# Kernel tuning notes

Hardware: AMD Instinct MI355X
Metric: run time of the kernel (lower is better)

Reference implementation:

```python
import jax, jax.numpy as jnp
import numpy as np

BN_EPS = 1e-5

def setup_inputs() -> dict:
    key = jax.random.key(0)
    ks = jax.random.split(key, 6)
    N, D, H = 1024, 256, 128
    scale = 0.05
    return {
        "graph_embeddings": jax.random.normal(ks[0], (N, D), jnp.float32),
        "W1": jax.random.normal(ks[1], (2 * D, H), jnp.float32) * scale,
        "b1": jnp.zeros((H,), jnp.float32),
        "W2": jax.random.normal(ks[2], (H, 1), jnp.float32) * scale,
        "b2": jnp.zeros((1,), jnp.float32),
        "Wg": jax.random.normal(ks[3], (D, H), jnp.float32) * scale,
        "bg": jnp.zeros((H,), jnp.float32),
        "gamma": jnp.ones((H,), jnp.float32),
        "beta": jnp.zeros((H,), jnp.float32),
    }

def reference(graph_embeddings, W1, b1, W2, b2, Wg, bg, gamma, beta):
    N, D = graph_embeddings.shape
    # Pairwise similarity MLP: sim(i,j) = sigmoid(W2 @ relu(W1 @ [x_i; x_j] + b1) + b2)
    # Split W1 over the concat dim so we never materialize [N,N,2D].
    a = graph_embeddings @ W1[:D]          # [N, H] contribution of x_i
    c = graph_embeddings @ W1[D:]          # [N, H] contribution of x_j
    h = jax.nn.relu(a[:, None, :] + c[None, :, :] + b1)   # [N, N, H]
    sim = jax.nn.sigmoid(jnp.einsum('ijh,h->ij', h, W2[:, 0]) + b2[0])  # [N, N]
    # Torch loop uses sim(i,j) with i<j for both directions; keep edge iff sim > 0.5.
    U = jnp.triu(sim, k=1)
    A = jnp.where(U > 0.5, U, 0.0)
    A = A + A.T + jnp.eye(N, dtype=sim.dtype)  # symmetric + GCN self-loops (weight 1)
    # GCN symmetric normalization: D^{-1/2} A D^{-1/2}
    deg = A.sum(axis=1)
    dis = jax.lax.rsqrt(deg)
    A_hat = A * dis[:, None] * dis[None, :]
    out = A_hat @ (graph_embeddings @ Wg) + bg  # [N, H]
    # BatchNorm1d (training mode: batch stats, biased variance)
    mean = out.mean(axis=0)
    var = out.var(axis=0)
    out = gamma * (out - mean) * jax.lax.rsqrt(var + BN_EPS) + beta
    return jax.nn.relu(out)
```

## Files before the change

kernel.cpp:

```cpp
#include <hip/hip_runtime.h>
#include <math.h>

constexpr int NN = 1024;
constexpr int DD = 256;
constexpr int HH = 128;
constexpr float BN_EPS = 1e-5f;

constexpr int OFF_A      = 0;
constexpr int OFF_AP     = OFF_A + NN * NN;
constexpr int OFF_CP     = OFF_AP + NN * HH;
constexpr int OFF_Y      = OFF_CP + NN * HH;
constexpr int OFF_DEG    = OFF_Y + NN * HH;
constexpr int OFF_STATS  = OFF_DEG + NN;
constexpr int OFF_OUTPRE = OFF_STATS + 256;

__global__ __launch_bounds__(256) void k1_gemm(
    const float* __restrict__ X, const float* __restrict__ W1,
    const float* __restrict__ Wg, const float* __restrict__ b1,
    float* __restrict__ aP, float* __restrict__ cP, float* __restrict__ Y,
    float* __restrict__ deg, float* __restrict__ stats) {
  const int tid = threadIdx.x;
  const int blk = blockIdx.x;
  if (blk >= 192) {
    if (blk == 192) {
      for (int i = tid; i < NN; i += 256) deg[i] = 0.f;
    } else {
      stats[tid] = 0.f;
    }
    return;
  }
  __shared__ float xs[16 * 256];
  __shared__ float ws[64 * 128];
  const int i0 = (blk & 63) * 16;
  const int m = blk >> 6;
  const float* W = (m == 0) ? W1 : (m == 1 ? W1 + DD * HH : Wg);
  const float* Xbase = X + i0 * DD;
#pragma unroll
  for (int v = 0; v < 4; ++v) {
    const int fi = (v * 256 + tid) * 4;
    *(float4*)(xs + fi) = *(const float4*)(Xbase + fi);
  }
  const int tx = tid & 31, ty = tid >> 5;
  float4 acc0 = make_float4(0.f, 0.f, 0.f, 0.f);
  float4 acc1 = make_float4(0.f, 0.f, 0.f, 0.f);
  for (int c = 0; c < 4; ++c) {
    __syncthreads();
    const float* Wbase = W + c * 64 * HH;
#pragma unroll
    for (int v = 0; v < 8; ++v) {
      const int fi = (v * 256 + tid) * 4;
      *(float4*)(ws + fi) = *(const float4*)(Wbase + fi);
    }
    __syncthreads();
    const float* xr0 = xs + (ty * 2) * 256 + c * 64;
    const float* xr1 = xs + (ty * 2 + 1) * 256 + c * 64;
#pragma unroll 4
    for (int d = 0; d < 64; d += 4) {
      const float4 x0 = *(const float4*)(xr0 + d);
      const float4 x1 = *(const float4*)(xr1 + d);
      const float4 w0 = *(const float4*)(ws + (d + 0) * 128 + tx * 4);
      const float4 w1 = *(const float4*)(ws + (d + 1) * 128 + tx * 4);
      const float4 w2 = *(const float4*)(ws + (d + 2) * 128 + tx * 4);
      const float4 w3 = *(const float4*)(ws + (d + 3) * 128 + tx * 4);
      acc0.x = fmaf(x0.x, w0.x, acc0.x); acc0.y = fmaf(x0.x, w0.y, acc0.y);
      acc0.z = fmaf(x0.x, w0.z, acc0.z); acc0.w = fmaf(x0.x, w0.w, acc0.w);
      acc1.x = fmaf(x1.x, w0.x, acc1.x); acc1.y = fmaf(x1.x, w0.y, acc1.y);
      acc1.z = fmaf(x1.x, w0.z, acc1.z); acc1.w = fmaf(x1.x, w0.w, acc1.w);
      acc0.x = fmaf(x0.y, w1.x, acc0.x); acc0.y = fmaf(x0.y, w1.y, acc0.y);
      acc0.z = fmaf(x0.y, w1.z, acc0.z); acc0.w = fmaf(x0.y, w1.w, acc0.w);
      acc1.x = fmaf(x1.y, w1.x, acc1.x); acc1.y = fmaf(x1.y, w1.y, acc1.y);
      acc1.z = fmaf(x1.y, w1.z, acc1.z); acc1.w = fmaf(x1.y, w1.w, acc1.w);
      acc0.x = fmaf(x0.z, w2.x, acc0.x); acc0.y = fmaf(x0.z, w2.y, acc0.y);
      acc0.z = fmaf(x0.z, w2.z, acc0.z); acc0.w = fmaf(x0.z, w2.w, acc0.w);
      acc1.x = fmaf(x1.z, w2.x, acc1.x); acc1.y = fmaf(x1.z, w2.y, acc1.y);
      acc1.z = fmaf(x1.z, w2.z, acc1.z); acc1.w = fmaf(x1.z, w2.w, acc1.w);
      acc0.x = fmaf(x0.w, w3.x, acc0.x); acc0.y = fmaf(x0.w, w3.y, acc0.y);
      acc0.z = fmaf(x0.w, w3.z, acc0.z); acc0.w = fmaf(x0.w, w3.w, acc0.w);
      acc1.x = fmaf(x1.w, w3.x, acc1.x); acc1.y = fmaf(x1.w, w3.y, acc1.y);
      acc1.z = fmaf(x1.w, w3.z, acc1.z); acc1.w = fmaf(x1.w, w3.w, acc1.w);
    }
  }
  float* dst = (m == 0) ? aP : (m == 1 ? cP : Y);
  if (m == 0) {
    const float4 bv = *(const float4*)(b1 + tx * 4);
    acc0.x += bv.x; acc0.y += bv.y; acc0.z += bv.z; acc0.w += bv.w;
    acc1.x += bv.x; acc1.y += bv.y; acc1.z += bv.z; acc1.w += bv.w;
  }
  const int r0 = i0 + ty * 2;
  *(float4*)(dst + r0 * HH + tx * 4) = acc0;
  *(float4*)(dst + (r0 + 1) * HH + tx * 4) = acc1;
}

__global__ __launch_bounds__(256) void k2_pairwise(
    const float* __restrict__ aP, const float* __restrict__ cP,
    const float* __restrict__ W2, const float* __restrict__ b2,
    float* __restrict__ A, float* __restrict__ deg) {
  __shared__ float as[32 * 132];
  __shared__ float cs[32 * 132];
  __shared__ float es[32 * 33];
  __shared__ float ws2[128];
  const int tid = threadIdx.x;
  int tt = blockIdx.x, ti = 0;
  while (tt >= 32 - ti) { tt -= 32 - ti; ++ti; }
  const int tj = ti + tt;
  const int i0 = ti * 32, j0 = tj * 32;
  if (tid < 32) *(float4*)(ws2 + tid * 4) = *(const float4*)(W2 + tid * 4);
  for (int idx = tid; idx < 32 * HH; idx += 256) {
    const int row = idx >> 7, col = idx & 127;
    as[row * 132 + col] = aP[(i0 + row) * HH + col];
    cs[row * 132 + col] = cP[(j0 + row) * HH + col];
  }
  __syncthreads();
  const int li0 = (tid >> 4) * 2, lj0 = (tid & 15) * 2;
  float s00 = 0.f, s01 = 0.f, s10 = 0.f, s11 = 0.f;
#pragma unroll 8
  for (int h = 0; h < HH; h += 4) {
    const float4 a0 = *(const float4*)(as + li0 * 132 + h);
    const float4 a1 = *(const float4*)(as + (li0 + 1) * 132 + h);
    const float4 c0 = *(const float4*)(cs + lj0 * 132 + h);
    const float4 c1 = *(const float4*)(cs + (lj0 + 1) * 132 + h);
    const float4 w = *(const float4*)(ws2 + h);
    s00 += fmaxf(a0.x + c0.x, 0.f) * w.x + fmaxf(a0.y + c0.y, 0.f) * w.y +
           fmaxf(a0.z + c0.z, 0.f) * w.z + fmaxf(a0.w + c0.w, 0.f) * w.w;
    s01 += fmaxf(a0.x + c1.x, 0.f) * w.x + fmaxf(a0.y + c1.y, 0.f) * w.y +
           fmaxf(a0.z + c1.z, 0.f) * w.z + fmaxf(a0.w + c1.w, 0.f) * w.w;
    s10 += fmaxf(a1.x + c0.x, 0.f) * w.x + fmaxf(a1.y + c0.y, 0.f) * w.y +
           fmaxf(a1.z + c0.z, 0.f) * w.z + fmaxf(a1.w + c0.w, 0.f) * w.w;
    s11 += fmaxf(a1.x + c1.x, 0.f) * w.x + fmaxf(a1.y + c1.y, 0.f) * w.y +
           fmaxf(a1.z + c1.z, 0.f) * w.z + fmaxf(a1.w + c1.w, 0.f) * w.w;
  }
  const float b2v = b2[0];
  auto edge = [b2v](float s) {
    s += b2v;
    return s > 0.f ? 1.f / (1.f + __expf(-s)) : 0.f;
  };
  es[(li0 + 0) * 33 + lj0 + 0] = edge(s00);
  es[(li0 + 0) * 33 + lj0 + 1] = edge(s01);
  es[(li0 + 1) * 33 + lj0 + 0] = edge(s10);
  es[(li0 + 1) * 33 + lj0 + 1] = edge(s11);
  __syncthreads();
  if (ti == tj) {
    float f[2][2];
#pragma unroll
    for (int r = 0; r < 2; ++r)
#pragma unroll
      for (int c = 0; c < 2; ++c) {
        const int li = li0 + r, lj = lj0 + c;
        f[r][c] =
            (li == lj) ? 1.f : (li < lj ? es[li * 33 + lj] : es[lj * 33 + li]);
      }
    __syncthreads();
    es[(li0 + 0) * 33 + lj0 + 0] = f[0][0];
    es[(li0 + 0) * 33 + lj0 + 1] = f[0][1];
    es[(li0 + 1) * 33 + lj0 + 0] = f[1][0];
    es[(li0 + 1) * 33 + lj0 + 1] = f[1][1];
    __syncthreads();
  }
  if (tid < 32) {
    float s = 0.f;
#pragma unroll
    for (int c = 0; c < 32; ++c) s += es[tid * 33 + c];
    atomicAdd(deg + i0 + tid, s);
  } else if (tid < 64 && ti != tj) {
    const int c = tid - 32;
    float s = 0.f;
#pragma unroll
    for (int r = 0; r < 32; ++r) s += es[r * 33 + c];
    atomicAdd(deg + j0 + c, s);
  }
#pragma unroll
  for (int r = 0; r < 2; ++r)
#pragma unroll
    for (int c = 0; c < 2; ++c) {
      const int li = li0 + r, lj = lj0 + c;
      A[(i0 + li) * NN + j0 + lj] = es[li * 33 + lj];
      if (ti != tj) A[(j0 + li) * NN + i0 + lj] = es[lj * 33 + li];
    }
}

__global__ __launch_bounds__(256) void k3_spmm(
    const float* __restrict__ A, const float* __restrict__ Y,
    const float* __restrict__ deg, const float* __restrict__ bg,
    float* __restrict__ out_pre, float* __restrict__ stats) {
  __shared__ float Ast[NN * 4];
  __shared__ float disl[NN];
  __shared__ float red[8 * 520];
  __shared__ float sm1[256], sm2[256];
  const int tid = threadIdx.x;
  const int i0 = blockIdx.x * 4;
  {
    const float4 dv = *(const float4*)(deg + tid * 4);
    float4 r;
    r.x = rsqrtf(dv.x); r.y = rsqrtf(dv.y);
    r.z = rsqrtf(dv.z); r.w = rsqrtf(dv.w);
    *(float4*)(disl + tid * 4) = r;
  }
  __syncthreads();
  const float* Ab = A + i0 * NN;
#pragma unroll
  for (int v = 0; v < 4; ++v) {
    const int fi = (v * 256 + tid) * 4;
    const float4 av = *(const float4*)(Ab + fi);
    const int r = fi >> 10, j = fi & 1023;
    Ast[(j + 0) * 4 + r] = av.x * disl[j + 0];
    Ast[(j + 1) * 4 + r] = av.y * disl[j + 1];
    Ast[(j + 2) * 4 + r] = av.z * disl[j + 2];
    Ast[(j + 3) * 4 + r] = av.w * disl[j + 3];
  }
  __syncthreads();
  const int tx = tid & 31, ty = tid >> 5;
  const int jbase = ty * 128;
  float4 acc[4];
#pragma unroll
  for (int r = 0; r < 4; ++r) acc[r] = make_float4(0.f, 0.f, 0.f, 0.f);
  const float* Yb = Y + jbase * HH + tx * 4;
#pragma unroll 4
  for (int jj = 0; jj < 128; ++jj) {
    const float4 yv = *(const float4*)(Yb + jj * HH);
    const float4 ab = *(const float4*)(Ast + (jbase + jj) * 4);
    acc[0].x = fmaf(ab.x, yv.x, acc[0].x); acc[0].y = fmaf(ab.x, yv.y, acc[0].y);
    acc[0].z = fmaf(ab.x, yv.z, acc[0].z); acc[0].w = fmaf(ab.x, yv.w, acc[0].w);
    acc[1].x = fmaf(ab.y, yv.x, acc[1].x); acc[1].y = fmaf(ab.y, yv.y, acc[1].y);
    acc[1].z = fmaf(ab.y, yv.z, acc[1].z); acc[1].w = fmaf(ab.y, yv.w, acc[1].w);
    acc[2].x = fmaf(ab.z, yv.x, acc[2].x); acc[2].y = fmaf(ab.z, yv.y, acc[2].y);
    acc[2].z = fmaf(ab.z, yv.z, acc[2].z); acc[2].w = fmaf(ab.z, yv.w, acc[2].w);
    acc[3].x = fmaf(ab.w, yv.x, acc[3].x); acc[3].y = fmaf(ab.w, yv.y, acc[3].y);
    acc[3].z = fmaf(ab.w, yv.z, acc[3].z); acc[3].w = fmaf(ab.w, yv.w, acc[3].w);
  }
#pragma unroll
  for (int r = 0; r < 4; ++r)
    *(float4*)(red + ty * 520 + r * 128 + tx * 4) = acc[r];
  __syncthreads();
  const int h = tid & 127, rr = tid >> 7;
  float v0 = 0.f, v1 = 0.f;
#pragma unroll
  for (int t = 0; t < 8; ++t) {
    v0 += red[t * 520 + rr * 128 + h];
    v1 += red[t * 520 + (rr + 2) * 128 + h];
  }
  const float bgv = bg[h];
  v0 = v0 * disl[i0 + rr] + bgv;
  v1 = v1 * disl[i0 + rr + 2] + bgv;
  out_pre[(i0 + rr) * HH + h] = v0;
  out_pre[(i0 + rr + 2) * HH + h] = v1;
  sm1[rr * 128 + h] = v0 + v1;
  sm2[rr * 128 + h] = v0 * v0 + v1 * v1;
  __syncthreads();
  if (rr == 0) {
    atomicAdd(&stats[h], sm1[h] + sm1[128 + h]);
    atomicAdd(&stats[128 + h], sm2[h] + sm2[128 + h]);
  }
}

__global__ __launch_bounds__(256) void k4_bn(
    const float* __restrict__ out_pre, const float* __restrict__ stats,
    const float* __restrict__ gamma, const float* __restrict__ beta,
    float* __restrict__ out) {
  const int idx = blockIdx.x * 256 + threadIdx.x;
  const int h = idx & 127;
  const float mean = stats[h] * (1.f / NN);
  const float var = stats[128 + h] * (1.f / NN) - mean * mean;
  float v = (out_pre[idx] - mean) * rsqrtf(var + BN_EPS);
  v = gamma[h] * v + beta[h];
  out[idx] = fmaxf(v, 0.f);
}

extern "C" void kernel_launch(void* const* d_in, const int* in_sizes, int n_in,
                              void* d_out, int out_size, void* d_ws,
                              size_t ws_size, hipStream_t stream) {
  const float* X = (const float*)d_in[0];
  const float* W1 = (const float*)d_in[1];
  const float* b1 = (const float*)d_in[2];
  const float* W2 = (const float*)d_in[3];
  const float* b2 = (const float*)d_in[4];
  const float* Wg = (const float*)d_in[5];
  const float* bg = (const float*)d_in[6];
  const float* gamma = (const float*)d_in[7];
  const float* beta = (const float*)d_in[8];
  float* out = (float*)d_out;

  float* w = (float*)d_ws;
  float* A = w + OFF_A;
  float* aP = w + OFF_AP;
  float* cP = w + OFF_CP;
  float* Y = w + OFF_Y;
  float* deg = w + OFF_DEG;
  float* stats = w + OFF_STATS;
  float* out_pre = w + OFF_OUTPRE;

  k1_gemm<<<dim3(194), 256, 0, stream>>>(X, W1, Wg, b1, aP, cP, Y, deg, stats);
  k2_pairwise<<<dim3(528), 256, 0, stream>>>(aP, cP, W2, b2, A, deg);
  k3_spmm<<<dim3(256), 256, 0, stream>>>(A, Y, deg, bg, out_pre, stats);
  k4_bn<<<dim3(512), 256, 0, stream>>>(out_pre, stats, gamma, beta, out);
}
```

Measured before the change: 117.5 us.

## Fuse BatchNorm into SpMM kernel via grid-wide atomic barrier

Removes the separate BN kernel and the out_pre intermediate buffer. The SpMM kernel now waits at a software grid barrier, an atomic counter spun on by one thread per block, until every block has added its column statistics. It then applies batch normalisation and ReLU to values still held in registers and writes the final output. This saves a kernel launch and a round trip of the intermediate through global memory. In exchange it requires all 256 blocks to be resident at once to avoid deadlock, and adds spin-wait latency.

```diff
diff --git a/kernel.cpp b/kernel.cpp
--- a/kernel.cpp
+++ b/kernel.cpp
@@ -12,18 +12,20 @@
 constexpr int OFF_Y      = OFF_CP + NN * HH;
 constexpr int OFF_DEG    = OFF_Y + NN * HH;
 constexpr int OFF_STATS  = OFF_DEG + NN;
-constexpr int OFF_OUTPRE = OFF_STATS + 256;
+constexpr int OFF_CTR    = OFF_STATS + 256;
 
 __global__ __launch_bounds__(256) void k1_gemm(
     const float* __restrict__ X, const float* __restrict__ W1,
     const float* __restrict__ Wg, const float* __restrict__ b1,
     float* __restrict__ aP, float* __restrict__ cP, float* __restrict__ Y,
-    float* __restrict__ deg, float* __restrict__ stats) {
+    float* __restrict__ deg, float* __restrict__ stats,
+    unsigned int* __restrict__ ctr) {
   const int tid = threadIdx.x;
   const int blk = blockIdx.x;
   if (blk >= 192) {
     if (blk == 192) {
       for (int i = tid; i < NN; i += 256) deg[i] = 0.f;
+      if (tid == 0) *ctr = 0u;
     } else {
       stats[tid] = 0.f;
     }
@@ -178,10 +180,12 @@
     }
 }
 
-__global__ __launch_bounds__(256) void k3_spmm(
+__global__ __launch_bounds__(256) void k3_spmm_bn(
     const float* __restrict__ A, const float* __restrict__ Y,
     const float* __restrict__ deg, const float* __restrict__ bg,
-    float* __restrict__ out_pre, float* __restrict__ stats) {
+    const float* __restrict__ gamma, const float* __restrict__ beta,
+    float* __restrict__ stats, unsigned int* __restrict__ ctr,
+    float* __restrict__ out) {
   __shared__ float Ast[NN * 4];
   __shared__ float disl[NN];
   __shared__ float red[8 * 520];
@@ -241,8 +245,6 @@
   const float bgv = bg[h];
   v0 = v0 * disl[i0 + rr] + bgv;
   v1 = v1 * disl[i0 + rr + 2] + bgv;
-  out_pre[(i0 + rr) * HH + h] = v0;
-  out_pre[(i0 + rr + 2) * HH + h] = v1;
   sm1[rr * 128 + h] = v0 + v1;
   sm2[rr * 128 + h] = v0 * v0 + v1 * v1;
   __syncthreads();
@@ -250,19 +252,28 @@
     atomicAdd(&stats[h], sm1[h] + sm1[128 + h]);
     atomicAdd(&stats[128 + h], sm2[h] + sm2[128 + h]);
   }
-}
-
-__global__ __launch_bounds__(256) void k4_bn(
-    const float* __restrict__ out_pre, const float* __restrict__ stats,
-    const float* __restrict__ gamma, const float* __restrict__ beta,
-    float* __restrict__ out) {
-  const int idx = blockIdx.x * 256 + threadIdx.x;
-  const int h = idx & 127;
-  const float mean = stats[h] * (1.f / NN);
-  const float var = stats[128 + h] * (1.f / NN) - mean * mean;
-  float v = (out_pre[idx] - mean) * rsqrtf(var + BN_EPS);
-  v = gamma[h] * v + beta[h];
-  out[idx] = fmaxf(v, 0.f);
+  __syncthreads();
+  if (tid == 0) {
+    __threadfence();
+    __hip_atomic_fetch_add(ctr, 1u, __ATOMIC_ACQ_REL, __HIP_MEMORY_SCOPE_AGENT);
+    while (__hip_atomic_load(ctr, __ATOMIC_ACQUIRE, __HIP_MEMORY_SCOPE_AGENT) <
+           256u) {
+      __builtin_amdgcn_s_sleep(2);
+    }
+  }
+  __syncthreads();
+  const float s1 =
+      __hip_atomic_load(&stats[h], __ATOMIC_ACQUIRE, __HIP_MEMORY_SCOPE_AGENT);
+  const float s2 = __hip_atomic_load(&stats[128 + h], __ATOMIC_ACQUIRE,
+                                     __HIP_MEMORY_SCOPE_AGENT);
+  const float mean = s1 * (1.f / NN);
+  const float var = s2 * (1.f / NN) - mean * mean;
+  const float istd = rsqrtf(var + BN_EPS);
+  const float g = gamma[h], b = beta[h];
+  v0 = (v0 - mean) * istd * g + b;
+  v1 = (v1 - mean) * istd * g + b;
+  out[(i0 + rr) * HH + h] = fmaxf(v0, 0.f);
+  out[(i0 + rr + 2) * HH + h] = fmaxf(v1, 0.f);
 }
 
 extern "C" void kernel_launch(void* const* d_in, const int* in_sizes, int n_in,
@@ -286,10 +297,11 @@
   float* Y = w + OFF_Y;
   float* deg = w + OFF_DEG;
   float* stats = w + OFF_STATS;
-  float* out_pre = w + OFF_OUTPRE;
-
-  k1_gemm<<<dim3(194), 256, 0, stream>>>(X, W1, Wg, b1, aP, cP, Y, deg, stats);
+  unsigned int* ctr = (unsigned int*)(w + OFF_CTR);
+
+  k1_gemm<<<dim3(194), 256, 0, stream>>>(X, W1, Wg, b1, aP, cP, Y, deg, stats,
+                                         ctr);
   k2_pairwise<<<dim3(528), 256, 0, stream>>>(aP, cP, W2, b2, A, deg);
-  k3_spmm<<<dim3(256), 256, 0, stream>>>(A, Y, deg, bg, out_pre, stats);
-  k4_bn<<<dim3(512), 256, 0, stream>>>(out_pre, stats, gamma, beta, out);
+  k3_spmm_bn<<<dim3(256), 256, 0, stream>>>(A, Y, deg, bg, gamma, beta, stats,
+                                            ctr, out);
 }
```

Result: slower. 144.6 us (+23.1%).
